# Kernel tuning notes

Measured on AMD Instinct MI355X. Metric: run time of the kernel, lower is better.

## Reference

```python
import jax, jax.numpy as jnp
import numpy as np

N, C = 4194304, 10
EPS = 1e-10
FOCAL_EPS = 1e-8
TEMP, THETA = 0.01, 0.1
NUM_TH = 21


def setup_inputs() -> dict:
    key = jax.random.key(0)
    k1, k2 = jax.random.split(key)
    logits = jax.random.normal(k1, (N, C), dtype=jnp.float32)
    probs = jax.nn.softmax(logits, axis=1)
    labels = jax.random.randint(k2, (N,), 0, C)
    y = jax.nn.one_hot(labels, C, dtype=jnp.float32)
    return {"probs": probs, "y": y}


def _soft_T(e):
    # sigmoid( (1/temp) * log( e*(1-theta) / clamp((1-e)*theta, eps) ) )
    num = e * (1.0 - THETA)
    den = jnp.maximum((1.0 - e) * THETA, EPS)
    frac = jnp.maximum(num / den, EPS)
    return jax.nn.sigmoid(jnp.log(frac) / TEMP)


def reference(probs, y):
    entmax = jnp.log(jnp.asarray(C, dtype=probs.dtype))
    predictions = jnp.argmax(probs, axis=1)             # [N]
    labels = jnp.argmax(y)                              # scalar (flattened argmax, as in torch code)

    # predictive uncertainty (type=0): entropy of probs per-sample
    unc = -jnp.sum(probs * jnp.log(jnp.maximum(probs, EPS)), axis=1)  # [N]

    th_list = jnp.linspace(0.0, 1.0, NUM_TH, dtype=probs.dtype)       # [21]
    umin, umax = jnp.min(unc), jnp.max(unc)
    unc_th = umin + th_list * (umax - umin)                           # [21]

    s = _soft_T(unc / entmax)                                         # [N]
    t = jnp.tanh(unc)                                                 # [N]
    w_cert = (1.0 - s) * (1.0 - t)   # weight when counted as 'certain'
    w_unc = s * t                    # weight when counted as 'uncertain'

    acc = (predictions == labels).astype(probs.dtype)                 # [N]
    inacc = 1.0 - acc

    le = (unc[None, :] <= unc_th[:, None]).astype(probs.dtype)        # [21, N]
    gt = 1.0 - le

    # one parallel masked-reduction pass over all 21 thresholds
    n_ac = le @ (acc * w_cert)
    n_au = gt @ (acc * w_unc)
    n_ic = le @ (inacc * w_cert)
    n_iu = gt @ (inacc * w_unc)

    avu = (n_ac + n_iu) / (n_ac + n_au + n_ic + n_iu + EPS)           # [21]

    # trapezoid rule over increasing th_list (direction = +1)
    dx = jnp.diff(th_list)
    auc_avu = jnp.sum((avu[1:] + avu[:-1]) * 0.5 * dx)

    # FocalLoss(gamma=1)
    logp = jnp.log(jnp.maximum(probs, FOCAL_EPS))
    ce_per = -jnp.sum(y * logp, axis=1)
    focal_per = -jnp.sum(y * logp * (1.0 - probs), axis=1)
    focal_loss = jnp.mean(focal_per)
    ce_loss = jnp.mean(ce_per)

    beta = 1.0
    savu_loss = -beta * jnp.log(jnp.maximum(auc_avu, EPS)) + focal_loss
    return (savu_loss, ce_loss)
```

## Files before the change

kernel.cpp:

```cpp
#include <hip/hip_runtime.h>

#define C 10
#define CHUNK_ROWS 128
#define CHUNK_FLOATS 1280
#define CHUNK_F4 320

typedef float f4_t __attribute__((ext_vector_type(4)));
typedef float f2_t __attribute__((ext_vector_type(2)));

__device__ __forceinline__ float waveSum(float v) {
#pragma unroll
  for (int o = 32; o > 0; o >>= 1) v += __shfl_down(v, o, 64);
  return v;
}
__device__ __forceinline__ float waveMin(float v) {
#pragma unroll
  for (int o = 32; o > 0; o >>= 1) v = fminf(v, __shfl_down(v, o, 64));
  return v;
}
__device__ __forceinline__ float waveMax(float v) {
#pragma unroll
  for (int o = 32; o > 0; o >>= 1) v = fmaxf(v, __shfl_down(v, o, 64));
  return v;
}
__device__ __forceinline__ unsigned waveMaxU(unsigned v) {
#pragma unroll
  for (int o = 32; o > 0; o >>= 1) {
    unsigned w = (unsigned)__shfl_down((int)v, o, 64);
    v = v > w ? v : w;
  }
  return v;
}

__global__ __launch_bounds__(128, 4) void pass1(
    const float4* __restrict__ probs4, const float4* __restrict__ y4,
    float2* __restrict__ us2,
    unsigned* __restrict__ uminInvSlots, unsigned* __restrict__ umaxSlots,
    float* __restrict__ ceSlots, float* __restrict__ focalSlots,
    int nchunks) {
  __shared__ float lds[2 * CHUNK_FLOATS];
  const int widx = threadIdx.x >> 6, lane = threadIdx.x & 63;
  f4_t* const bufP = (f4_t*)(lds + widx * CHUNK_FLOATS);

  const int gw = blockIdx.x * 2 + widx;
  const int NW = gridDim.x * 2;

  int label0 = 0;
  {
    const float* yf = (const float*)y4;
    float m = yf[0];
#pragma unroll
    for (int c = 1; c < C; ++c) {
      float v = yf[c];
      if (v > m) { m = v; label0 = c; }
    }
  }

  f4_t P[5], Y[5];
  auto issue = [&](int c) {
    const f4_t* gp = (const f4_t*)probs4 + (size_t)c * CHUNK_F4 + lane;
    const f4_t* gy = (const f4_t*)y4 + (size_t)c * CHUNK_F4 + lane;
#pragma unroll
    for (int q = 0; q < 5; ++q) {
      P[q] = gp[q * 64];
      Y[q] = gy[q * 64];
    }
  };

  float ceA = 0.f, foA = 0.f;
  float mnA = __uint_as_float(0x7f800000u), mxA = 0.f;

  if (gw < nchunks) issue(gw);
  for (int c = gw; c < nchunks; c += NW) {
#pragma unroll
    for (int q = 0; q < 5; ++q) {
      f4_t pv = P[q], yv = Y[q];
      float lpx = __logf(fmaxf(pv.x, 1e-10f));
      float lpy = __logf(fmaxf(pv.y, 1e-10f));
      float lpz = __logf(fmaxf(pv.z, 1e-10f));
      float lpw = __logf(fmaxf(pv.w, 1e-10f));
      float tx = yv.x * fmaxf(lpx, -18.420681f);
      float ty = yv.y * fmaxf(lpy, -18.420681f);
      float tz = yv.z * fmaxf(lpz, -18.420681f);
      float tw = yv.w * fmaxf(lpw, -18.420681f);
      ceA -= tx + ty + tz + tw;
      foA -= tx * (1.f - pv.x) + ty * (1.f - pv.y) + tz * (1.f - pv.z) +
             tw * (1.f - pv.w);
      bufP[q * 64 + lane] = pv;
    }

    if (c + NW < nchunks) issue(c + NW);

    float u0 = 0.f, u1 = 0.f;
    float m0 = -1.f, m1 = -1.f;
    int am0 = 0, am1 = 0;
#pragma unroll
    for (int q = 0; q < 5; ++q) {
      f4_t v = bufP[lane * 5 + q];
      float vv[4] = {v.x, v.y, v.z, v.w};
#pragma unroll
      for (int j = 0; j < 4; ++j) {
        int e = 4 * q + j;
        float p = vv[j];
        float lp = __logf(fmaxf(p, 1e-10f));
        if (e < 10) {
          u0 -= p * lp;
          if (p > m0) { m0 = p; am0 = e; }
        } else {
          u1 -= p * lp;
          if (p > m1) { m1 = p; am1 = e - 10; }
        }
      }
    }
    mnA = fminf(mnA, fminf(u0, u1));
    mxA = fmaxf(mxA, fmaxf(u0, u1));

    unsigned s0 = __float_as_uint(u0) | ((am0 == label0) ? 0u : 0x80000000u);
    unsigned s1 = __float_as_uint(u1) | ((am1 == label0) ? 0u : 0x80000000u);
    f2_t o;
    o.x = __uint_as_float(s0);
    o.y = __uint_as_float(s1);
    __builtin_nontemporal_store(o, (f2_t*)&us2[(size_t)c * 64 + lane]);
  }

  float ce = waveSum(ceA), fo = waveSum(foA);
  float mn = waveMin(mnA), mx = waveMax(mxA);
  if (lane == 0) {
    int slot = gw & 63;
    atomicAdd(&ceSlots[slot], ce);
    atomicAdd(&focalSlots[slot], fo);
    atomicMax(&uminInvSlots[slot], ~__float_as_uint(mn));
    atomicMax(&umaxSlots[slot], __float_as_uint(mx));
  }
}

__global__ __launch_bounds__(256, 4) void pass2(
    const float4* __restrict__ us4, int n4,
    const unsigned* __restrict__ uminInvSlots, const unsigned* __restrict__ umaxSlots,
    float* __restrict__ ghist) {
  __shared__ float hist[88 * 64];
  __shared__ float smm[2];
  const int tid = threadIdx.x, lane = tid & 63;
  for (int i = tid; i < 88 * 64; i += 256) hist[i] = 0.f;
  if (tid < 64) {
    unsigned mnInv = waveMaxU(uminInvSlots[tid]);
    unsigned mxb = waveMaxU(umaxSlots[tid]);
    if (tid == 0) { smm[0] = __uint_as_float(~mnInv); smm[1] = __uint_as_float(mxb); }
  }
  __syncthreads();
  const float umin = smm[0], delta = smm[1] - smm[0];
  float th[21];
#pragma unroll
  for (int k = 0; k < 21; ++k) th[k] = fmaf(0.05f * (float)k, delta, umin);

  const int stride = gridDim.x * 256;
  for (int i = blockIdx.x * 256 + tid; i < n4; i += stride) {
    f4_t v = __builtin_nontemporal_load((const f4_t*)us4 + i);
    float vv[4] = {v.x, v.y, v.z, v.w};
#pragma unroll
    for (int q = 0; q < 4; ++q) {
      unsigned b = __float_as_uint(vv[q]);
      int rb = (b >> 31) ? 44 : 0;
      float u = __uint_as_float(b & 0x7fffffffu);
      float e = u * 0.4342944819f;
      float lnum = __logf(e * 0.9f);
      float lden = __logf(fmaxf((1.f - e) * 0.1f, 1e-10f));
      float x = fmaxf(lnum - lden, -23.0258509f) * 100.f;
      float s = __builtin_amdgcn_rcpf(1.f + __expf(-x));
      float t = 1.f - 2.f * __builtin_amdgcn_rcpf(__expf(2.f * u) + 1.f);
      float wc = (1.f - s) * (1.f - t), wu = s * t;
      int j = 0;
#pragma unroll
      for (int k = 0; k < 21; ++k) j += (u > th[k]) ? 1 : 0;
      atomicAdd(&hist[(rb + j) * 64 + lane], wc);
      atomicAdd(&hist[(rb + 22 + j) * 64 + lane], wu);
    }
  }
  __syncthreads();
#pragma unroll
  for (int st = 32; st >= 1; st >>= 1) {
    for (int idx = tid; idx < 88 * st; idx += 256) {
      int r = idx / st, c = idx - r * st;
      hist[r * 64 + c] += hist[r * 64 + c + st];
    }
    __syncthreads();
  }
  int slot = blockIdx.x & 63;
  for (int r = tid; r < 88; r += 256)
    atomicAdd(&ghist[slot * 88 + r], hist[r * 64]);
}

__global__ __launch_bounds__(256) void pass3(
    const float* __restrict__ ghist,
    const float* __restrict__ ceSlots, const float* __restrict__ focalSlots,
    float* __restrict__ out, float invN) {
  __shared__ float hr[96];
  __shared__ float scf[2];
  int tid = threadIdx.x;
  if (tid < 88) {
    float s = 0.f;
    for (int q = 0; q < 64; ++q) s += ghist[q * 88 + tid];
    hr[tid] = s;
  }
  if (tid >= 128 && tid < 192) {
    int l = tid - 128;
    float ce = waveSum(ceSlots[l]);
    float fo = waveSum(focalSlots[l]);
    if (l == 0) { scf[0] = ce; scf[1] = fo; }
  }
  __syncthreads();
  if (tid == 0) {
    float totAU = 0.f, totIU = 0.f;
    for (int j = 0; j < 22; ++j) { totAU += hr[22 + j]; totIU += hr[66 + j]; }
    float n_ac = 0.f, n_ic = 0.f, n_au = totAU, n_iu = totIU;
    float auc = 0.f, prev = 0.f;
    for (int k = 0; k < 21; ++k) {
      n_ac += hr[k]; n_ic += hr[44 + k];
      n_au -= hr[22 + k]; n_iu -= hr[66 + k];
      float avu = (n_ac + n_iu) / (n_ac + n_au + n_ic + n_iu + 1e-10f);
      if (k > 0) auc += (avu + prev) * 0.5f * 0.05f;
      prev = avu;
    }
    out[0] = -logf(fmaxf(auc, 1e-10f)) + scf[1] * invN;
    out[1] = scf[0] * invN;
  }
}

extern "C" void kernel_launch(void* const* d_in, const int* in_sizes, int n_in,
                              void* d_out, int out_size, void* d_ws, size_t ws_size,
                              hipStream_t stream) {
  const float* probs = (const float*)d_in[0];
  const float* y = (const float*)d_in[1];
  float* out = (float*)d_out;
  const int N = in_sizes[0] / C;

  float* wsf = (float*)d_ws;
  unsigned* uminInvSlots = (unsigned*)wsf;
  unsigned* umaxSlots = (unsigned*)(wsf + 64);
  float* ceSlots = wsf + 128;
  float* focalSlots = wsf + 192;
  float* ghist = wsf + 256;
  float* us = wsf + 5888;

  hipMemsetAsync(d_ws, 0, 5888 * sizeof(float), stream);

  const int nchunks = N / CHUNK_ROWS;
  float invN = 1.0f / (float)N;

  pass1<<<4096, 128, 0, stream>>>((const float4*)probs, (const float4*)y,
                                  (float2*)us, uminInvSlots, umaxSlots,
                                  ceSlots, focalSlots, nchunks);
  pass2<<<1024, 256, 0, stream>>>((const float4*)us, N / 4, uminInvSlots,
                                  umaxSlots, ghist);
  pass3<<<1, 256, 0, stream>>>(ghist, ceSlots, focalSlots, out, invN);
}
```

Baseline: 395.9 us.

## Replace LDS-staged chunk loads with per-thread row-pair direct loads in pass1

Pass1 no longer loads coalesced 128-row chunks per wave and transposes them through LDS. Instead, each thread reads its own pair of rows (five contiguous float4 from probs and from y) with nontemporal loads and does the CE/focal sums in the same loop as the entropy and argmax. This removes the LDS round-trip, the software prefetch, and the LDS allocation, and raises the occupancy hint to 8. The cost is per-lane strided 80-byte accesses that are less coalesced per instruction, and the loss of explicit load/compute overlap.

After: 588.4 us. +48.6%, slower.

```diff
diff --git a/kernel.cpp b/kernel.cpp
--- a/kernel.cpp
+++ b/kernel.cpp
@@ -1,9 +1,6 @@
 #include <hip/hip_runtime.h>
 
 #define C 10
-#define CHUNK_ROWS 128
-#define CHUNK_FLOATS 1280
-#define CHUNK_F4 320
 
 typedef float f4_t __attribute__((ext_vector_type(4)));
 typedef float f2_t __attribute__((ext_vector_type(2)));
@@ -32,18 +29,17 @@
   return v;
 }
 
-__global__ __launch_bounds__(128, 4) void pass1(
+__global__ __launch_bounds__(128, 8) void pass1(
     const float4* __restrict__ probs4, const float4* __restrict__ y4,
     float2* __restrict__ us2,
     unsigned* __restrict__ uminInvSlots, unsigned* __restrict__ umaxSlots,
     float* __restrict__ ceSlots, float* __restrict__ focalSlots,
-    int nchunks) {
-  __shared__ float lds[2 * CHUNK_FLOATS];
-  const int widx = threadIdx.x >> 6, lane = threadIdx.x & 63;
-  f4_t* const bufP = (f4_t*)(lds + widx * CHUNK_FLOATS);
-
-  const int gw = blockIdx.x * 2 + widx;
-  const int NW = gridDim.x * 2;
+    int npairs) {
+  const int t = blockIdx.x * 128 + threadIdx.x;
+  const int T = gridDim.x * 128;
+  const int lane = threadIdx.x & 63;
+  const f4_t* bp = (const f4_t*)probs4;
+  const f4_t* by = (const f4_t*)y4;
 
   int label0 = 0;
   {
@@ -56,53 +52,34 @@
     }
   }
 
-  f4_t P[5], Y[5];
-  auto issue = [&](int c) {
-    const f4_t* gp = (const f4_t*)probs4 + (size_t)c * CHUNK_F4 + lane;
-    const f4_t* gy = (const f4_t*)y4 + (size_t)c * CHUNK_F4 + lane;
-#pragma unroll
-    for (int q = 0; q < 5; ++q) {
-      P[q] = gp[q * 64];
-      Y[q] = gy[q * 64];
-    }
-  };
-
   float ceA = 0.f, foA = 0.f;
   float mnA = __uint_as_float(0x7f800000u), mxA = 0.f;
 
-  if (gw < nchunks) issue(gw);
-  for (int c = gw; c < nchunks; c += NW) {
+  for (int pi = t; pi < npairs; pi += T) {
+    f4_t P[5], Y[5];
+    const f4_t* gp = bp + (size_t)pi * 5;
+    const f4_t* gy = by + (size_t)pi * 5;
 #pragma unroll
     for (int q = 0; q < 5; ++q) {
-      f4_t pv = P[q], yv = Y[q];
-      float lpx = __logf(fmaxf(pv.x, 1e-10f));
-      float lpy = __logf(fmaxf(pv.y, 1e-10f));
-      float lpz = __logf(fmaxf(pv.z, 1e-10f));
-      float lpw = __logf(fmaxf(pv.w, 1e-10f));
-      float tx = yv.x * fmaxf(lpx, -18.420681f);
-      float ty = yv.y * fmaxf(lpy, -18.420681f);
-      float tz = yv.z * fmaxf(lpz, -18.420681f);
-      float tw = yv.w * fmaxf(lpw, -18.420681f);
-      ceA -= tx + ty + tz + tw;
-      foA -= tx * (1.f - pv.x) + ty * (1.f - pv.y) + tz * (1.f - pv.z) +
-             tw * (1.f - pv.w);
-      bufP[q * 64 + lane] = pv;
-    }
-
-    if (c + NW < nchunks) issue(c + NW);
+      P[q] = __builtin_nontemporal_load(gp + q);
+      Y[q] = __builtin_nontemporal_load(gy + q);
+    }
 
     float u0 = 0.f, u1 = 0.f;
     float m0 = -1.f, m1 = -1.f;
     int am0 = 0, am1 = 0;
 #pragma unroll
     for (int q = 0; q < 5; ++q) {
-      f4_t v = bufP[lane * 5 + q];
-      float vv[4] = {v.x, v.y, v.z, v.w};
+      float pv[4] = {P[q].x, P[q].y, P[q].z, P[q].w};
+      float yv[4] = {Y[q].x, Y[q].y, Y[q].z, Y[q].w};
 #pragma unroll
       for (int j = 0; j < 4; ++j) {
-        int e = 4 * q + j;
-        float p = vv[j];
+        const int e = 4 * q + j;
+        float p = pv[j];
         float lp = __logf(fmaxf(p, 1e-10f));
+        float te = yv[j] * fmaxf(lp, -18.420681f);
+        ceA -= te;
+        foA -= te * (1.f - p);
         if (e < 10) {
           u0 -= p * lp;
           if (p > m0) { m0 = p; am0 = e; }
@@ -120,13 +97,13 @@
     f2_t o;
     o.x = __uint_as_float(s0);
     o.y = __uint_as_float(s1);
-    __builtin_nontemporal_store(o, (f2_t*)&us2[(size_t)c * 64 + lane]);
+    __builtin_nontemporal_store(o, (f2_t*)&us2[pi]);
   }
 
   float ce = waveSum(ceA), fo = waveSum(foA);
   float mn = waveMin(mnA), mx = waveMax(mxA);
   if (lane == 0) {
-    int slot = gw & 63;
+    int slot = (t >> 6) & 63;
     atomicAdd(&ceSlots[slot], ce);
     atomicAdd(&focalSlots[slot], fo);
     atomicMax(&uminInvSlots[slot], ~__float_as_uint(mn));
@@ -244,12 +221,12 @@
 
   hipMemsetAsync(d_ws, 0, 5888 * sizeof(float), stream);
 
-  const int nchunks = N / CHUNK_ROWS;
+  const int npairs = N / 2;
   float invN = 1.0f / (float)N;
 
   pass1<<<4096, 128, 0, stream>>>((const float4*)probs, (const float4*)y,
                                   (float2*)us, uminInvSlots, umaxSlots,
-                                  ceSlots, focalSlots, nchunks);
+                                  ceSlots, focalSlots, npairs);
   pass2<<<1024, 256, 0, stream>>>((const float4*)us, N / 4, uminInvSlots,
                                   umaxSlots, ghist);
   pass3<<<1, 256, 0, stream>>>(ghist, ceSlots, focalSlots, out, invN);
```
